# Optimization experiments

Hardware: AMD Instinct MI355X
Metric: run time of the kernel (lower is better)

Reference implementation:

```python
import jax, jax.numpy as jnp
import numpy as np

B, L, D, H = 4, 4096, 1024, 16
HD = D // H  # head_dim = 64
SCALE = 1.0 / np.sqrt(HD)


def setup_inputs() -> dict:
    key = jax.random.key(0)
    ks = jax.random.split(key, 6)
    x = jax.random.normal(ks[0], (B, L, D), dtype=jnp.float32)
    Wqkv_w = jax.random.normal(ks[1], (3 * D, D), dtype=jnp.float32) * (1.0 / np.sqrt(D))
    Wqkv_b = jax.random.normal(ks[2], (3 * D,), dtype=jnp.float32) * 0.02
    out_w = jax.random.normal(ks[3], (D, D), dtype=jnp.float32) * (1.0 / np.sqrt(D))
    out_b = jax.random.normal(ks[4], (D,), dtype=jnp.float32) * 0.02
    gamma_raw = jax.random.uniform(ks[5], (H,), dtype=jnp.float32, minval=0.0, maxval=2.0)
    return {"x": x, "Wqkv_w": Wqkv_w, "Wqkv_b": Wqkv_b,
            "out_w": out_w, "out_b": out_b, "gamma_raw": gamma_raw}


def reference(x, Wqkv_w, Wqkv_b, out_w, out_b, gamma_raw):
    b, l, dm = x.shape
    # qkv projection: [B, L, 3*D] -> [3, B, H, L, hd]
    qkv = x @ Wqkv_w.T + Wqkv_b
    qkv = qkv.reshape(b, l, 3, H, HD).transpose(2, 0, 3, 1, 4)
    q, k, v = qkv[0], qkv[1], qkv[2]      # each [B, H, L, hd]
    k = k * SCALE
    g = jax.nn.sigmoid(gamma_raw)          # [H]
    gb = g[None, :, None, None]            # broadcast over [B, H, hd, hd]

    # move time axis to front for scan: [L, B, H, hd]
    qT = q.transpose(2, 0, 1, 3)
    kT = k.transpose(2, 0, 1, 3)
    vT = v.transpose(2, 0, 1, 3)

    def step(state, qkv_t):
        q_t, k_t, v_t = qkv_t
        # S = gamma * S + v k^T
        state = gb * state + jnp.einsum('bhi,bhj->bhij', v_t, k_t)
        # y = S q
        y_t = jnp.einsum('bhij,bhj->bhi', state, q_t)
        return state, y_t

    state0 = jnp.zeros((b, H, HD, HD), dtype=x.dtype)
    _, y = jax.lax.scan(step, state0, (qT, kT, vT))  # y: [L, B, H, hd]

    y = y.transpose(1, 0, 2, 3).reshape(b, l, dm)    # [B, L, D]
    return y @ out_w.T + out_b
```

## Files before the change

### kernel.cpp

```cpp
#include <hip/hip_runtime.h>
#include <cstdint>
#include <cstddef>

#define B_    4
#define L_    4096
#define D_    1024
#define H_    16
#define HD_   64
#define ND3_  3072
#define M1_   16384
#define NCH_  64
#define CSZ_  64
#define SCALE_ 0.125f

typedef __attribute__((ext_vector_type(8))) __bf16 bf16x8;
typedef __attribute__((ext_vector_type(4))) float f32x4;
typedef __attribute__((ext_vector_type(4))) unsigned int uint4v;

__device__ __forceinline__ float u2f(unsigned int u) { return __builtin_bit_cast(float, u); }
__device__ __forceinline__ unsigned int f2u(float f) { return __builtin_bit_cast(unsigned int, f); }
__device__ __forceinline__ float bf2f(unsigned short s) { return u2f(((unsigned int)s) << 16); }
__device__ __forceinline__ unsigned short f2bf(float f) {
  unsigned int u = f2u(f);
  u = u + 0x7fffu + ((u >> 16) & 1u);
  return (unsigned short)(u >> 16);
}

__device__ __forceinline__ void glds16(const unsigned short* g, unsigned short* l) {
  __builtin_amdgcn_global_load_lds(
      (const __attribute__((address_space(1))) void*)(uintptr_t)g,
      (__attribute__((address_space(3))) void*)(uintptr_t)l, 16, 0, 0);
}

__global__ __launch_bounds__(256) void cast_kernel(const float* __restrict__ in,
                                                   unsigned short* __restrict__ out, int n)
{
  int i = (blockIdx.x * 256 + threadIdx.x) * 4;
  if (i + 3 < n) {
    float4 f = *(const float4*)(in + i);
    out[i + 0] = f2bf(f.x);
    out[i + 1] = f2bf(f.y);
    out[i + 2] = f2bf(f.z);
    out[i + 3] = f2bf(f.w);
  }
}

template<int EPI, int BM, int BN, int WM, int WN, int THREADS>
__global__ __launch_bounds__(THREADS, (THREADS == 512 ? 2 : 3))
void gemm_pipe(const unsigned short* __restrict__ A, const unsigned short* __restrict__ Bm,
               const float* __restrict__ bias,
               unsigned short* __restrict__ qo, unsigned short* __restrict__ ko,
               unsigned short* __restrict__ vo,
               float* __restrict__ Co, int M, int N, int K)
{
  constexpr int TR = THREADS / 4;
  constexpr int AR = BM / TR;
  constexpr int BRR = BN / TR;
  constexpr int FM = BM / WM / 16;
  constexpr int FN = BN / WN / 16;
  constexpr int ASZ = BM * 32, BSZ = BN * 32;

  __shared__ __align__(16) unsigned short Ab[3 * ASZ];
  __shared__ __align__(16) unsigned short Bb[3 * BSZ];

  const int nwg = gridDim.x;
  const int wg = (blockIdx.x & 7) * (nwg >> 3) + (blockIdx.x >> 3);
  const int nbn = N / BN;
  const int bm = wg / nbn, bn = wg - bm * nbn;
  const int m0 = bm * BM, n0 = bn * BN;
  const int tid = threadIdx.x;
  const int lane = tid & 63, wid = tid >> 6;
  const int wr = wid / WN, wc = wid % WN;
  const int fl = lane & 15, fh = lane >> 4;

  const int rowbase = wid * 16 + (lane >> 2);
  const int ckst = (lane & 3) ^ ((rowbase & 3) ^ ((rowbase >> 2) & 3));
  const int ckrd = fh ^ ((fl & 3) ^ ((fl >> 2) & 3));

  const int nt = K >> 5;

  f32x4 acc[FM][FN] = {};

  auto stageA = [&](int kt, int d) {
#pragma unroll
    for (int s = 0; s < AR; ++s)
      glds16(A + (size_t)(m0 + s * TR + rowbase) * K + kt * 32 + ckst * 8,
             Ab + d * ASZ + s * TR * 32 + wid * 512);
  };
  auto stageB = [&](int kt, int d) {
#pragma unroll
    for (int s = 0; s < BRR; ++s)
      glds16(Bm + (size_t)(n0 + s * TR + rowbase) * K + kt * 32 + ckst * 8,
             Bb + d * BSZ + s * TR * 32 + wid * 512);
  };

  stageA(0, 0); stageB(0, 0);
  stageA(1, 1); stageB(1, 1);

  for (int t = 0; t < nt; ++t) {
    const int d = t % 3;
    if (t < nt - 1) { asm volatile("s_waitcnt vmcnt(4)" ::: "memory"); }
    else            { asm volatile("s_waitcnt vmcnt(0)" ::: "memory"); }
    __builtin_amdgcn_s_barrier();
    __builtin_amdgcn_sched_barrier(0);

    const unsigned short* Abuf = Ab + d * ASZ;
    const unsigned short* Bbuf = Bb + d * BSZ;

    bf16x8 bfrag[FN], afrag[FM / 2];
#pragma unroll
    for (int n = 0; n < FN; ++n)
      bfrag[n] = *(const bf16x8*)(Bbuf + (wc * (BN / WN) + n * 16 + fl) * 32 + ckrd * 8);
#pragma unroll
    for (int m = 0; m < FM / 2; ++m)
      afrag[m] = *(const bf16x8*)(Abuf + (wr * (BM / WM) + m * 16 + fl) * 32 + ckrd * 8);
    if (t + 2 < nt) stageA(t + 2, (t + 2) % 3);
    asm volatile("s_waitcnt lgkmcnt(0)" ::: "memory");
    __builtin_amdgcn_sched_barrier(0);
    __builtin_amdgcn_s_setprio(1);
#pragma unroll
    for (int m = 0; m < FM / 2; ++m)
#pragma unroll
      for (int n = 0; n < FN; ++n)
        acc[m][n] = __builtin_amdgcn_mfma_f32_16x16x32_bf16(afrag[m], bfrag[n], acc[m][n], 0, 0, 0);
    __builtin_amdgcn_s_setprio(0);

    bf16x8 afrag2[FM / 2];
#pragma unroll
    for (int m = 0; m < FM / 2; ++m)
      afrag2[m] = *(const bf16x8*)(Abuf + (wr * (BM / WM) + (m + FM / 2) * 16 + fl) * 32 + ckrd * 8);
    if (t + 2 < nt) stageB(t + 2, (t + 2) % 3);
    asm volatile("s_waitcnt lgkmcnt(0)" ::: "memory");
    __builtin_amdgcn_sched_barrier(0);
    __builtin_amdgcn_s_setprio(1);
#pragma unroll
    for (int m = 0; m < FM / 2; ++m)
#pragma unroll
      for (int n = 0; n < FN; ++n)
        acc[m + FM / 2][n] = __builtin_amdgcn_mfma_f32_16x16x32_bf16(afrag2[m], bfrag[n], acc[m + FM / 2][n], 0, 0, 0);
    __builtin_amdgcn_s_setprio(0);
  }

  const int rb = fh << 2;
#pragma unroll
  for (int m = 0; m < FM; ++m) {
#pragma unroll
    for (int n = 0; n < FN; ++n) {
#pragma unroll
      for (int r = 0; r < 4; ++r) {
        int row = m0 + wr * (BM / WM) + m * 16 + rb + r;
        int col = n0 + wc * (BN / WN) + n * 16 + fl;
        float val = acc[m][n][r] + bias[col];
        if constexpr (EPI == 0) {
          int which = col >> 10;
          int hh = (col >> 6) & 15;
          int hd = col & 63;
          int bb = row >> 12;
          int tt = row & 4095;
          size_t idx = (((size_t)(bb * H_ + hh)) * L_ + tt) * HD_ + hd;
          if (which == 0)      qo[idx] = f2bf(val);
          else if (which == 1) ko[idx] = f2bf(val * SCALE_);
          else                 vo[idx] = f2bf(val);
        } else {
          Co[(size_t)row * N + col] = val;
        }
      }
    }
  }
}

__global__ __launch_bounds__(256) void ret_phase1(
    const unsigned short* __restrict__ kb, const unsigned short* __restrict__ vb,
    const float* __restrict__ gamma_raw, unsigned short* __restrict__ Sbuf)
{
  int bhc = blockIdx.x;
  int c = bhc & 63, bh = bhc >> 6, h = bh & 15;
  float g = 1.f / (1.f + expf(-gamma_raw[h]));
  float lg2g = log2f(g);

  __shared__ __align__(16) unsigned short Kt[64][72];
  __shared__ __align__(16) unsigned short Vwt[64][72];

  int tid = threadIdx.x;
  size_t base = ((size_t)bh * L_ + (size_t)c * CSZ_) * HD_;
#pragma unroll
  for (int qq = 0; qq < 16; ++qq) {
    int e = tid + qq * 256;
    int j = e >> 6, col = e & 63;
    float wj = exp2f(lg2g * (float)(63 - j));
    Kt[col][j] = kb[base + e];
    Vwt[col][j] = f2bf(bf2f(vb[base + e]) * wj);
  }
  __syncthreads();

  int lane = tid & 63, w = tid >> 6;
  int fl = lane & 15, fh = lane >> 4;

  bf16x8 av0 = *(const bf16x8*)(&Vwt[w * 16 + fl][fh * 8]);
  bf16x8 av1 = *(const bf16x8*)(&Vwt[w * 16 + fl][32 + fh * 8]);

  int rb = fh << 2;
  unsigned short* out = Sbuf + (size_t)bhc * 4096;
#pragma unroll
  for (int jf = 0; jf < 4; ++jf) {
    bf16x8 bk0 = *(const bf16x8*)(&Kt[jf * 16 + fl][fh * 8]);
    bf16x8 bk1 = *(const bf16x8*)(&Kt[jf * 16 + fl][32 + fh * 8]);
    f32x4 z = {};
    z = __builtin_amdgcn_mfma_f32_16x16x32_bf16(av0, bk0, z, 0, 0, 0);
    z = __builtin_amdgcn_mfma_f32_16x16x32_bf16(av1, bk1, z, 0, 0, 0);
#pragma unroll
    for (int r = 0; r < 4; ++r) {
      int a = w * 16 + rb + r, bcol = jf * 16 + fl;
      out[a * 64 + bcol] = f2bf(z[r]);
    }
  }
}

__global__ __launch_bounds__(256) void ret_phase2(unsigned short* __restrict__ Sbuf,
                                                  const float* __restrict__ gamma_raw)
{
  int bh = blockIdx.x >> 3, grp = blockIdx.x & 7;
  int h = bh & 15;
  float g = 1.f / (1.f + expf(-gamma_raw[h]));
  float gC = powf(g, 64.f);
  int e = (grp * 256 + threadIdx.x) * 2;
  unsigned short* base = Sbuf + (size_t)bh * (NCH_ * 4096) + e;
  float s0 = 0.f, s1 = 0.f;
  for (int c = 0; c < NCH_; ++c) {
    unsigned int u = *(unsigned int*)(base + (size_t)c * 4096);
    float a0 = bf2f((unsigned short)(u & 0xffffu));
    float a1 = bf2f((unsigned short)(u >> 16));
    *(unsigned int*)(base + (size_t)c * 4096) =
        (unsigned int)f2bf(s0) | ((unsigned int)f2bf(s1) << 16);
    s0 = gC * s0 + a0;
    s1 = gC * s1 + a1;
  }
}

__global__ __launch_bounds__(256) void ret_phase3(
    const unsigned short* __restrict__ qb, const unsigned short* __restrict__ kb,
    const unsigned short* __restrict__ vb, const unsigned short* __restrict__ Sbuf,
    const float* __restrict__ gamma_raw, unsigned short* __restrict__ y)
{
  int bhc = blockIdx.x;
  int c = bhc & 63, bh = bhc >> 6, h = bh & 15, b = bh >> 4;
  float g = 1.f / (1.f + expf(-gamma_raw[h]));
  float lg2g = log2f(g);

  __shared__ __align__(16) unsigned short Qs[64][72];
  __shared__ __align__(16) unsigned short Ks[64][72];
  __shared__ __align__(16) unsigned short Vt[64][72];
  __shared__ __align__(16) unsigned short Sb[64][72];
  __shared__ __align__(16) unsigned short Ps[64][72];

  int tid = threadIdx.x;
  size_t base = ((size_t)bh * L_ + (size_t)c * CSZ_) * HD_;
  const unsigned short* Sp = Sbuf + (size_t)bhc * 4096;
#pragma unroll
  for (int qq = 0; qq < 16; ++qq) {
    int e = tid + qq * 256;
    int r = e >> 6, col = e & 63;
    Qs[r][col] = qb[base + e];
    Ks[r][col] = kb[base + e];
    Vt[col][r] = vb[base + e];
    Sb[r][col] = Sp[e];
  }
  __syncthreads();

  int lane = tid & 63, w = tid >> 6;
  int fl = lane & 15, fh = lane >> 4;
  int rb = fh << 2;

  bf16x8 aq0 = *(const bf16x8*)(&Qs[w * 16 + fl][fh * 8]);
  bf16x8 aq1 = *(const bf16x8*)(&Qs[w * 16 + fl][32 + fh * 8]);

  f32x4 pc[4], acc[4];
#pragma unroll
  for (int jf = 0; jf < 4; ++jf) {
    bf16x8 bk0 = *(const bf16x8*)(&Ks[jf * 16 + fl][fh * 8]);
    bf16x8 bk1 = *(const bf16x8*)(&Ks[jf * 16 + fl][32 + fh * 8]);
    f32x4 z = {};
    z = __builtin_amdgcn_mfma_f32_16x16x32_bf16(aq0, bk0, z, 0, 0, 0);
    z = __builtin_amdgcn_mfma_f32_16x16x32_bf16(aq1, bk1, z, 0, 0, 0);
    pc[jf] = z;

    bf16x8 bs0 = *(const bf16x8*)(&Sb[jf * 16 + fl][fh * 8]);
    bf16x8 bs1 = *(const bf16x8*)(&Sb[jf * 16 + fl][32 + fh * 8]);
    f32x4 zz = {};
    zz = __builtin_amdgcn_mfma_f32_16x16x32_bf16(aq0, bs0, zz, 0, 0, 0);
    zz = __builtin_amdgcn_mfma_f32_16x16x32_bf16(aq1, bs1, zz, 0, 0, 0);
    acc[jf] = zz;
  }

#pragma unroll
  for (int jf = 0; jf < 4; ++jf) {
#pragma unroll
    for (int r = 0; r < 4; ++r) {
      int i = w * 16 + rb + r, j = jf * 16 + fl;
      float val = (j <= i) ? pc[jf][r] * exp2f(lg2g * (float)(i - j)) : 0.f;
      Ps[i][j] = f2bf(val);
    }
  }

  float gi1[4];
#pragma unroll
  for (int r = 0; r < 4; ++r) gi1[r] = exp2f(lg2g * (float)(w * 16 + rb + r + 1));
#pragma unroll
  for (int jf = 0; jf < 4; ++jf)
#pragma unroll
    for (int r = 0; r < 4; ++r) acc[jf][r] *= gi1[r];

  __syncthreads();

  bf16x8 ap0 = *(const bf16x8*)(&Ps[w * 16 + fl][fh * 8]);
  bf16x8 ap1 = *(const bf16x8*)(&Ps[w * 16 + fl][32 + fh * 8]);
#pragma unroll
  for (int jf = 0; jf < 4; ++jf) {
    bf16x8 bv0 = *(const bf16x8*)(&Vt[jf * 16 + fl][fh * 8]);
    bf16x8 bv1 = *(const bf16x8*)(&Vt[jf * 16 + fl][32 + fh * 8]);
    acc[jf] = __builtin_amdgcn_mfma_f32_16x16x32_bf16(ap0, bv0, acc[jf], 0, 0, 0);
    acc[jf] = __builtin_amdgcn_mfma_f32_16x16x32_bf16(ap1, bv1, acc[jf], 0, 0, 0);
  }

  size_t yrow = ((size_t)(b * L_ + c * CSZ_)) * D_ + h * HD_;
#pragma unroll
  for (int jf = 0; jf < 4; ++jf) {
#pragma unroll
    for (int r = 0; r < 4; ++r) {
      int i = w * 16 + rb + r;
      y[yrow + (size_t)i * D_ + jf * 16 + fl] = f2bf(acc[jf][r]);
    }
  }
}

extern "C" void kernel_launch(void* const* d_in, const int* in_sizes, int n_in,
                              void* d_out, int out_size, void* d_ws, size_t ws_size,
                              hipStream_t stream)
{
  const float* x        = (const float*)d_in[0];
  const float* Wqkv_w   = (const float*)d_in[1];
  const float* Wqkv_b   = (const float*)d_in[2];
  const float* out_w    = (const float*)d_in[3];
  const float* out_b    = (const float*)d_in[4];
  const float* gamma_raw= (const float*)d_in[5];
  float* out = (float*)d_out;

  char* ws = (char*)d_ws;
  unsigned short* x_bf    = (unsigned short*)ws; ws += (size_t)16777216 * 2;
  unsigned short* wqkv_bf = (unsigned short*)ws; ws += (size_t)3145728 * 2;
  unsigned short* wout_bf = (unsigned short*)ws; ws += (size_t)1048576 * 2;
  unsigned short* qb      = (unsigned short*)ws; ws += (size_t)16777216 * 2;
  unsigned short* kb      = (unsigned short*)ws; ws += (size_t)16777216 * 2;
  unsigned short* vb      = (unsigned short*)ws; ws += (size_t)16777216 * 2;
  unsigned short* Sbuf    = (unsigned short*)ws; ws += (size_t)16777216 * 2;
  unsigned short* yb      = (unsigned short*)ws; ws += (size_t)16777216 * 2;

  cast_kernel<<<16384, 256, 0, stream>>>(x, x_bf, 16777216);
  cast_kernel<<<3072, 256, 0, stream>>>(Wqkv_w, wqkv_bf, 3145728);
  cast_kernel<<<1024, 256, 0, stream>>>(out_w, wout_bf, 1048576);

  gemm_pipe<0, 256, 256, 2, 4, 512><<<64 * 12, 512, 0, stream>>>(
      x_bf, wqkv_bf, Wqkv_b, qb, kb, vb, nullptr, M1_, ND3_, D_);

  ret_phase1<<<4096, 256, 0, stream>>>(kb, vb, gamma_raw, Sbuf);
  ret_phase2<<<512, 256, 0, stream>>>(Sbuf, gamma_raw);
  ret_phase3<<<4096, 256, 0, stream>>>(qb, kb, vb, Sbuf, gamma_raw, yb);

  gemm_pipe<1, 128, 128, 2, 2, 256><<<128 * 8, 256, 0, stream>>>(
      yb, wout_bf, out_b, nullptr, nullptr, nullptr, out, M1_, D_, D_);
}
```

Before: 243.8 us.

## Load GEMM B-operand directly into registers, bypassing LDS staging

The GEMM kernel no longer stages the weight (B) tile through shared memory. Each wave now loads its B fragments straight from global memory into double-buffered registers one k-step ahead, while A keeps the triple-buffered LDS pipeline. The tile-to-block mapping is changed to iterate M fastest, so blocks sharing a weight column are co-scheduled. The output projection moves to 256x256 tiles with 512 threads. This cuts LDS traffic and footprint, at the cost of more redundant global or L2 reads of B across waves, higher register pressure, and fewer blocks (256) for the second GEMM.

After: 317.3 us. 30.1% more time.

```diff
diff --git a/kernel.cpp b/kernel.cpp
--- a/kernel.cpp
+++ b/kernel.cpp
@@ -46,8 +46,8 @@
 }
 
 template<int EPI, int BM, int BN, int WM, int WN, int THREADS>
-__global__ __launch_bounds__(THREADS, (THREADS == 512 ? 2 : 3))
-void gemm_pipe(const unsigned short* __restrict__ A, const unsigned short* __restrict__ Bm,
+__global__ __launch_bounds__(THREADS, 2)
+void gemm_breg(const unsigned short* __restrict__ A, const unsigned short* __restrict__ Bm,
                const float* __restrict__ bias,
                unsigned short* __restrict__ qo, unsigned short* __restrict__ ko,
                unsigned short* __restrict__ vo,
@@ -55,18 +55,16 @@
 {
   constexpr int TR = THREADS / 4;
   constexpr int AR = BM / TR;
-  constexpr int BRR = BN / TR;
   constexpr int FM = BM / WM / 16;
   constexpr int FN = BN / WN / 16;
-  constexpr int ASZ = BM * 32, BSZ = BN * 32;
+  constexpr int ASZ = BM * 32;
 
   __shared__ __align__(16) unsigned short Ab[3 * ASZ];
-  __shared__ __align__(16) unsigned short Bb[3 * BSZ];
 
   const int nwg = gridDim.x;
   const int wg = (blockIdx.x & 7) * (nwg >> 3) + (blockIdx.x >> 3);
-  const int nbn = N / BN;
-  const int bm = wg / nbn, bn = wg - bm * nbn;
+  const int nbm = M / BM;
+  const int bm = wg % nbm, bn = wg / nbm;
   const int m0 = bm * BM, n0 = bn * BN;
   const int tid = threadIdx.x;
   const int lane = tid & 63, wid = tid >> 6;
@@ -81,40 +79,48 @@
 
   f32x4 acc[FM][FN] = {};
 
+  const unsigned short* bp[FN];
+#pragma unroll
+  for (int n = 0; n < FN; ++n)
+    bp[n] = Bm + (size_t)(n0 + wc * (BN / WN) + n * 16 + fl) * K + fh * 8;
+
   auto stageA = [&](int kt, int d) {
 #pragma unroll
     for (int s = 0; s < AR; ++s)
       glds16(A + (size_t)(m0 + s * TR + rowbase) * K + kt * 32 + ckst * 8,
              Ab + d * ASZ + s * TR * 32 + wid * 512);
   };
-  auto stageB = [&](int kt, int d) {
-#pragma unroll
-    for (int s = 0; s < BRR; ++s)
-      glds16(Bm + (size_t)(n0 + s * TR + rowbase) * K + kt * 32 + ckst * 8,
-             Bb + d * BSZ + s * TR * 32 + wid * 512);
-  };
-
-  stageA(0, 0); stageB(0, 0);
-  stageA(1, 1); stageB(1, 1);
-
-  for (int t = 0; t < nt; ++t) {
-    const int d = t % 3;
-    if (t < nt - 1) { asm volatile("s_waitcnt vmcnt(4)" ::: "memory"); }
+
+  uint4v rB0[FN], rB1[FN];
+
+  stageA(0, 0);
+  __builtin_amdgcn_sched_barrier(0);
+#pragma unroll
+  for (int n = 0; n < FN; ++n) rB0[n] = *(const uint4v*)(bp[n]);
+  __builtin_amdgcn_sched_barrier(0);
+  stageA(1, 1);
+  __builtin_amdgcn_sched_barrier(0);
+
+  auto iter = [&](int t, uint4v (&rcur)[FN], uint4v (&rnxt)[FN]) {
+    if (t < nt - 1) { asm volatile("s_waitcnt vmcnt(2)" ::: "memory"); }
     else            { asm volatile("s_waitcnt vmcnt(0)" ::: "memory"); }
     __builtin_amdgcn_s_barrier();
     __builtin_amdgcn_sched_barrier(0);
 
-    const unsigned short* Abuf = Ab + d * ASZ;
-    const unsigned short* Bbuf = Bb + d * BSZ;
-
-    bf16x8 bfrag[FN], afrag[FM / 2];
-#pragma unroll
-    for (int n = 0; n < FN; ++n)
-      bfrag[n] = *(const bf16x8*)(Bbuf + (wc * (BN / WN) + n * 16 + fl) * 32 + ckrd * 8);
+    const unsigned short* Abuf = Ab + (t % 3) * ASZ;
+
+    if (t + 1 < nt) {
+#pragma unroll
+      for (int n = 0; n < FN; ++n)
+        rnxt[n] = *(const uint4v*)(bp[n] + (size_t)(t + 1) * 32);
+    }
+    bf16x8 afrag[FM / 2];
 #pragma unroll
     for (int m = 0; m < FM / 2; ++m)
       afrag[m] = *(const bf16x8*)(Abuf + (wr * (BM / WM) + m * 16 + fl) * 32 + ckrd * 8);
+    __builtin_amdgcn_sched_barrier(0);
     if (t + 2 < nt) stageA(t + 2, (t + 2) % 3);
+    __builtin_amdgcn_sched_barrier(0);
     asm volatile("s_waitcnt lgkmcnt(0)" ::: "memory");
     __builtin_amdgcn_sched_barrier(0);
     __builtin_amdgcn_s_setprio(1);
@@ -122,14 +128,14 @@
     for (int m = 0; m < FM / 2; ++m)
 #pragma unroll
       for (int n = 0; n < FN; ++n)
-        acc[m][n] = __builtin_amdgcn_mfma_f32_16x16x32_bf16(afrag[m], bfrag[n], acc[m][n], 0, 0, 0);
+        acc[m][n] = __builtin_amdgcn_mfma_f32_16x16x32_bf16(
+            afrag[m], __builtin_bit_cast(bf16x8, rcur[n]), acc[m][n], 0, 0, 0);
     __builtin_amdgcn_s_setprio(0);
 
     bf16x8 afrag2[FM / 2];
 #pragma unroll
     for (int m = 0; m < FM / 2; ++m)
       afrag2[m] = *(const bf16x8*)(Abuf + (wr * (BM / WM) + (m + FM / 2) * 16 + fl) * 32 + ckrd * 8);
-    if (t + 2 < nt) stageB(t + 2, (t + 2) % 3);
     asm volatile("s_waitcnt lgkmcnt(0)" ::: "memory");
     __builtin_amdgcn_sched_barrier(0);
     __builtin_amdgcn_s_setprio(1);
@@ -137,8 +143,14 @@
     for (int m = 0; m < FM / 2; ++m)
 #pragma unroll
       for (int n = 0; n < FN; ++n)
-        acc[m + FM / 2][n] = __builtin_amdgcn_mfma_f32_16x16x32_bf16(afrag2[m], bfrag[n], acc[m + FM / 2][n], 0, 0, 0);
+        acc[m + FM / 2][n] = __builtin_amdgcn_mfma_f32_16x16x32_bf16(
+            afrag2[m], __builtin_bit_cast(bf16x8, rcur[n]), acc[m + FM / 2][n], 0, 0, 0);
     __builtin_amdgcn_s_setprio(0);
+  };
+
+  for (int tt = 0; tt < nt; tt += 2) {
+    iter(tt + 0, rB0, rB1);
+    iter(tt + 1, rB1, rB0);
   }
 
   const int rb = fh << 2;
@@ -156,8 +168,8 @@
           int hh = (col >> 6) & 15;
           int hd = col & 63;
           int bb = row >> 12;
-          int tt = row & 4095;
-          size_t idx = (((size_t)(bb * H_ + hh)) * L_ + tt) * HD_ + hd;
+          int tt2 = row & 4095;
+          size_t idx = (((size_t)(bb * H_ + hh)) * L_ + tt2) * HD_ + hd;
           if (which == 0)      qo[idx] = f2bf(val);
           else if (which == 1) ko[idx] = f2bf(val * SCALE_);
           else                 vo[idx] = f2bf(val);
@@ -359,13 +371,13 @@
   cast_kernel<<<3072, 256, 0, stream>>>(Wqkv_w, wqkv_bf, 3145728);
   cast_kernel<<<1024, 256, 0, stream>>>(out_w, wout_bf, 1048576);
 
-  gemm_pipe<0, 256, 256, 2, 4, 512><<<64 * 12, 512, 0, stream>>>(
+  gemm_breg<0, 256, 256, 2, 4, 512><<<64 * 12, 512, 0, stream>>>(
       x_bf, wqkv_bf, Wqkv_b, qb, kb, vb, nullptr, M1_, ND3_, D_);
 
   ret_phase1<<<4096, 256, 0, stream>>>(kb, vb, gamma_raw, Sbuf);
   ret_phase2<<<512, 256, 0, stream>>>(Sbuf, gamma_raw);
   ret_phase3<<<4096, 256, 0, stream>>>(qb, kb, vb, Sbuf, gamma_raw, yb);
 
-  gemm_pipe<1, 128, 128, 2, 2, 256><<<128 * 8, 256, 0, stream>>>(
+  gemm_breg<1, 256, 256, 2, 4, 512><<<64 * 4, 512, 0, stream>>>(
       yb, wout_bf, out_b, nullptr, nullptr, nullptr, out, M1_, D_, D_);
 }
```
